# Kernel optimization log

Measured on AMD Instinct MI355X. Metric: run time of the kernel, lower is better.

Reference implementation:

```python
import jax, jax.numpy as jnp
import numpy as np

N = 100000
E = 1600000
E_OUT = 400000
IN_DIM = 16
HID = 64
OUT_DIM = 2
L = 6
BN_EPS = 1e-5


def setup_inputs() -> dict:
    key = jax.random.key(0)
    ks = jax.random.split(key, 12)
    x = jax.random.normal(ks[0], (N, IN_DIM), dtype=jnp.float32)
    edge_index = jax.random.randint(ks[1], (2, E), 0, N, dtype=jnp.int64)
    edge_index_out = jax.random.randint(ks[2], (2, E_OUT), 0, N, dtype=jnp.int64)
    s_emb = 1.0 / np.sqrt(IN_DIM)
    s_hid = 1.0 / np.sqrt(HID)
    W_emb = jax.random.uniform(ks[3], (IN_DIM, HID), jnp.float32, -s_emb, s_emb)
    b_emb = jax.random.uniform(ks[4], (HID,), jnp.float32, -s_emb, s_emb)
    conv_W = jax.random.uniform(ks[5], (L, HID, HID), jnp.float32, -s_hid, s_hid)
    conv_b = jnp.zeros((L, HID), jnp.float32)
    bn_gamma = jnp.ones((L, HID), jnp.float32)
    bn_beta = jnp.zeros((L, HID), jnp.float32)
    s_fc = 1.0 / np.sqrt(2 * HID)
    fc_W = jax.random.uniform(ks[6], (2 * HID, OUT_DIM), jnp.float32, -s_fc, s_fc)
    fc_b = jax.random.uniform(ks[7], (OUT_DIM,), jnp.float32, -s_fc, s_fc)
    return dict(x=x, edge_index=edge_index, edge_index_out=edge_index_out,
                W_emb=W_emb, b_emb=b_emb, conv_W=conv_W, conv_b=conv_b,
                bn_gamma=bn_gamma, bn_beta=bn_beta, fc_W=fc_W, fc_b=fc_b)


def gcn_conv(h, W, b, src, dst, norm):
    # PyG GCNConv: h' = scatter_add(norm * (hW)[src] -> dst) + b
    hw = h @ W                                   # [N, HID]
    msgs = hw[src] * norm[:, None]               # [E+N, HID] gather
    agg = jax.ops.segment_sum(msgs, dst, num_segments=N)
    return agg + b


def batchnorm_train(h, gamma, beta):
    mean = jnp.mean(h, axis=0)
    var = jnp.mean(jnp.square(h - mean), axis=0)  # biased var (BN training)
    return (h - mean) * jax.lax.rsqrt(var + BN_EPS) * gamma + beta


def reference(x, edge_index, edge_index_out, W_emb, b_emb, conv_W, conv_b,
              bn_gamma, bn_beta, fc_W, fc_b):
    # add self-loops + symmetric normalization (computed once, shared by layers)
    loop = jnp.arange(N, dtype=edge_index.dtype)
    src = jnp.concatenate([edge_index[0], loop])
    dst = jnp.concatenate([edge_index[1], loop])
    deg = jax.ops.segment_sum(jnp.ones_like(dst, dtype=jnp.float32), dst, num_segments=N)
    dinv = jnp.where(deg > 0, jax.lax.rsqrt(jnp.maximum(deg, 1.0)), 0.0)
    norm = dinv[src] * dinv[dst]

    x_embed = x @ W_emb + b_emb                  # node embedding [N, HID]
    for i in range(L):
        h = gcn_conv(x_embed, conv_W[i], conv_b[i], src, dst, norm)
        h = jax.nn.relu(batchnorm_train(h, bn_gamma[i], bn_beta[i]))
        x_embed = x_embed + h                    # residual

    e_src, e_dst = edge_index_out[0], edge_index_out[1]
    edge_repr = jnp.concatenate([x_embed[e_src], x_embed[e_dst]], axis=-1)  # [E_out, 2*HID]
    return edge_repr @ fc_W + fc_b
```

## Files before the change

kernel.cpp:

```cpp
#include <hip/hip_runtime.h>

#define NN 100000
#define NE 1600000
#define NEO 400000
#define HID 64
#define NL 6
#define BN_EPS 1e-5f

#define SPMM_BLOCKS 6250
#define SCAN_BS 512
#define SCAN_NB 196
#define GRP_ROWS 12500

#define BIN_CHUNK 1024
#define BIN_J (BIN_CHUNK / 256)
#define BIN_BLOCKS ((NE + BIN_CHUNK - 1) / BIN_CHUNK)
#define BIN_CAP 210000
#define B2_BPG 98
#define H2_BPG 98

#define OFF_ECOL 0
#define OFF_XE   NE
#define OFF_AGG  (OFF_XE + NN * 32)
#define OFF_HWB  (OFF_AGG + NN * 32)

#define OD_DINV   0
#define OD_ROWPTR 100352
#define OD_CC     200704
#define OD_BSUM   300704
#define OD_SS     300960
#define OD_SUMS   301088
#define OD_GCUR   309280

typedef __attribute__((ext_vector_type(8))) short bf16x8;
typedef __attribute__((ext_vector_type(4))) float f32x4;

static __device__ __forceinline__ unsigned short f2bf(float f) {
    unsigned u = __float_as_uint(f);
    unsigned r = (u + 0x7FFF + ((u >> 16) & 1)) >> 16;
    return (unsigned short)r;
}
static __device__ __forceinline__ float bflo(unsigned u) {
    return __uint_as_float(u << 16);
}
static __device__ __forceinline__ float bfhi(unsigned u) {
    return __uint_as_float(u & 0xFFFF0000u);
}

__global__ void k_bin(const int* __restrict__ src, const int* __restrict__ dst,
                      int* __restrict__ gcur,
                      int* __restrict__ bsrc, int* __restrict__ bdst) {
    __shared__ int cw[4][8], bw[4][8], ow[4][8];
    int t = threadIdx.x;
    int w = t >> 6;
    if (t < 32) { ((int*)cw)[t] = 0; ((int*)ow)[t] = 0; }
    __syncthreads();
    int cb = blockIdx.x * BIN_CHUNK;
    int s[BIN_J], d[BIN_J], g[BIN_J];
#pragma unroll
    for (int j = 0; j < BIN_J; j++) {
        int e = cb + t + j * 256;
        s[j] = (e < NE) ? src[e] : -1;
        d[j] = (e < NE) ? dst[e] : -1;
        if (d[j] >= 0) {
            g[j] = (unsigned)d[j] / GRP_ROWS;
            atomicAdd(&cw[w][g[j]], 1);
        }
    }
    __syncthreads();
    if (t < 8) {
        int c0 = cw[0][t], c1 = cw[1][t], c2 = cw[2][t], c3 = cw[3][t];
        int base = t * BIN_CAP + atomicAdd(&gcur[t], c0 + c1 + c2 + c3);
        bw[0][t] = base;
        bw[1][t] = base + c0;
        bw[2][t] = base + c0 + c1;
        bw[3][t] = base + c0 + c1 + c2;
    }
    __syncthreads();
#pragma unroll
    for (int j = 0; j < BIN_J; j++) {
        if (d[j] >= 0) {
            int pos = bw[w][g[j]] + atomicAdd(&ow[w][g[j]], 1);
            bsrc[pos] = s[j];
            bdst[pos] = d[j];
        }
    }
}

__global__ void k_hist2(const int* __restrict__ gcur, const int* __restrict__ bdst,
                        int* __restrict__ cnt) {
    int g = blockIdx.x & 7;
    int b = blockIdx.x >> 3;
    int n = gcur[g];
    int base = g * BIN_CAP;
    for (int i = b * blockDim.x + threadIdx.x; i < n; i += H2_BPG * blockDim.x)
        atomicAdd(&cnt[bdst[base + i]], 1);
}

__global__ void k_scanA(const int* __restrict__ cnt, int* __restrict__ rowptr,
                        int* __restrict__ bsum, float* __restrict__ dinv) {
    __shared__ int sh[SCAN_BS];
    int t = threadIdx.x;
    int i = blockIdx.x * SCAN_BS + t;
    int v = (i < NN) ? cnt[i] : 0;
    sh[t] = v;
    __syncthreads();
    for (int off = 1; off < SCAN_BS; off <<= 1) {
        int a = (t >= off) ? sh[t - off] : 0;
        __syncthreads();
        sh[t] += a;
        __syncthreads();
    }
    if (i < NN) {
        rowptr[i] = sh[t] - v;
        dinv[i] = rsqrtf((float)(v + 1));
    }
    if (t == SCAN_BS - 1) bsum[blockIdx.x] = sh[t];
}

__global__ void k_scanB(int* __restrict__ bsum) {
    __shared__ int sh[256];
    int t = threadIdx.x;
    int v = (t < SCAN_NB) ? bsum[t] : 0;
    sh[t] = v;
    __syncthreads();
    for (int off = 1; off < 256; off <<= 1) {
        int a = (t >= off) ? sh[t - off] : 0;
        __syncthreads();
        sh[t] += a;
        __syncthreads();
    }
    if (t < SCAN_NB) bsum[t] = (t == 0) ? 0 : sh[t - 1];
}

__global__ void k_scanC(int* __restrict__ rowptr, const int* __restrict__ bsum,
                        int* __restrict__ cursor) {
    int i = blockIdx.x * SCAN_BS + threadIdx.x;
    if (i < NN) {
        int rp = rowptr[i] + bsum[blockIdx.x];
        rowptr[i] = rp;
        cursor[i] = rp;
    }
    if (i == 0) rowptr[NN] = NE;
}

__global__ void k_build2(const int* __restrict__ gcur, const int* __restrict__ bsrc,
                         const int* __restrict__ bdst, int* __restrict__ cursor,
                         int* __restrict__ ecol) {
    int g = blockIdx.x & 7;
    int b = blockIdx.x >> 3;
    int n = gcur[g];
    int base = g * BIN_CAP;
    for (int i = b * blockDim.x + threadIdx.x; i < n; i += B2_BPG * blockDim.x) {
        int d = bdst[base + i];
        int s = bsrc[base + i];
        int pos = atomicAdd(&cursor[d], 1);
        ecol[pos] = s;
    }
}

__global__ void k_embed(const float* __restrict__ x, const float* __restrict__ W,
                        const float* __restrict__ b, unsigned short* __restrict__ xe16) {
    __shared__ float Ws[16 * 64];
    __shared__ float bs[64];
    int t = threadIdx.x;
    for (int i = t; i < 16 * 64; i += 256) Ws[i] = W[i];
    if (t < 64) bs[t] = b[t];
    __syncthreads();
    int c = t & 63, r = t >> 6;
    int n0 = blockIdx.x * 64;
    for (int n = n0 + r; n < n0 + 64 && n < NN; n += 4) {
        const float* xr = x + n * 16;
        float acc = bs[c];
#pragma unroll
        for (int k = 0; k < 16; k++) acc = fmaf(xr[k], Ws[k * 64 + c], acc);
        xe16[(size_t)n * 64 + c] = f2bf(acc);
    }
}

__global__ void k_hw(unsigned short* __restrict__ xe16,
                     const float* __restrict__ W, const float* __restrict__ dinv,
                     const unsigned short* __restrict__ agg16,
                     const float* __restrict__ gamma, const float* __restrict__ beta,
                     const double* __restrict__ sumsPrev, double* __restrict__ sumsCur,
                     unsigned short* __restrict__ hwb, int apply) {
    __shared__ unsigned short Wt[64 * 72];
    __shared__ unsigned short Xb[64 * 72];
    __shared__ float sss[128];
    int t = threadIdx.x;
    int n0 = blockIdx.x * 64;
    if (blockIdx.x == 0) {
        for (int i = t; i < 2048; i += 256) sumsCur[i] = 0.0;
    }
    if (apply && t < 64) {
        double s = 0.0, q = 0.0;
#pragma unroll
        for (int k = 0; k < 16; k++) {
            s += sumsPrev[k * 128 + t];
            q += sumsPrev[k * 128 + 64 + t];
        }
        double mean = s / (double)NN;
        double var = q / (double)NN - mean * mean;
        float sc = gamma[t] * rsqrtf((float)var + BN_EPS);
        sss[t] = sc;
        sss[64 + t] = beta[t] - (float)mean * sc;
    }

    {
        int c = t & 63, r = t >> 6;
#pragma unroll
        for (int jj = 0; jj < 4; jj++) {
            float w0 = W[(r * 16 + jj * 4 + 0) * 64 + c];
            float w1 = W[(r * 16 + jj * 4 + 1) * 64 + c];
            float w2 = W[(r * 16 + jj * 4 + 2) * 64 + c];
            float w3 = W[(r * 16 + jj * 4 + 3) * 64 + c];
            uint2 pk;
            pk.x = ((unsigned)f2bf(w1) << 16) | f2bf(w0);
            pk.y = ((unsigned)f2bf(w3) << 16) | f2bf(w2);
            *(uint2*)&Wt[c * 72 + r * 16 + jj * 4] = pk;
        }
    }
    __syncthreads();

    {
        int n = t >> 2, kq = t & 3;
        int node = n0 + n;
        unsigned xs[8] = {0, 0, 0, 0, 0, 0, 0, 0};
        if (node < NN) {
            const uint4* xr = (const uint4*)(xe16 + (size_t)node * 64 + kq * 16);
            uint4 x0 = xr[0], x1 = xr[1];
            xs[0] = x0.x; xs[1] = x0.y; xs[2] = x0.z; xs[3] = x0.w;
            xs[4] = x1.x; xs[5] = x1.y; xs[6] = x1.z; xs[7] = x1.w;
            if (apply) {
                const uint4* ar = (const uint4*)(agg16 + (size_t)node * 64 + kq * 16);
                uint4 a0 = ar[0], a1 = ar[1];
                unsigned as[8] = {a0.x, a0.y, a0.z, a0.w, a1.x, a1.y, a1.z, a1.w};
                int c = kq * 16;
#pragma unroll
                for (int i = 0; i < 8; i++) {
                    float v0 = bflo(xs[i]) +
                               fmaxf(fmaf(bflo(as[i]), sss[c + 2 * i], sss[64 + c + 2 * i]), 0.f);
                    float v1 = bfhi(xs[i]) +
                               fmaxf(fmaf(bfhi(as[i]), sss[c + 2 * i + 1], sss[64 + c + 2 * i + 1]), 0.f);
                    xs[i] = ((unsigned)f2bf(v1) << 16) | f2bf(v0);
                }
                uint4* xw = (uint4*)(xe16 + (size_t)node * 64 + kq * 16);
                xw[0] = make_uint4(xs[0], xs[1], xs[2], xs[3]);
                xw[1] = make_uint4(xs[4], xs[5], xs[6], xs[7]);
            }
        }
        *(uint4*)&Xb[n * 72 + kq * 16] = make_uint4(xs[0], xs[1], xs[2], xs[3]);
        *(uint4*)&Xb[n * 72 + kq * 16 + 8] = make_uint4(xs[4], xs[5], xs[6], xs[7]);
    }
    __syncthreads();

    int lane = t & 63, w = t >> 6;
    int m = lane & 15, quad = lane >> 4;
    f32x4 acc[4];
#pragma unroll
    for (int tc = 0; tc < 4; tc++) acc[tc] = (f32x4){0.f, 0.f, 0.f, 0.f};
#pragma unroll
    for (int s = 0; s < 2; s++) {
        bf16x8 bfr = *(const bf16x8*)&Xb[(w * 16 + m) * 72 + s * 32 + quad * 8];
#pragma unroll
        for (int tc = 0; tc < 4; tc++) {
            bf16x8 afr = *(const bf16x8*)&Wt[(tc * 16 + m) * 72 + s * 32 + quad * 8];
            acc[tc] = __builtin_amdgcn_mfma_f32_16x16x32_bf16(afr, bfr, acc[tc], 0, 0, 0);
        }
    }
    int node = n0 + w * 16 + m;
    if (node < NN) {
        float di = dinv[node];
#pragma unroll
        for (int tc = 0; tc < 4; tc++) {
            int c0 = tc * 16 + quad * 4;
            uint2 pk;
            pk.x = ((unsigned)f2bf(acc[tc][1] * di) << 16) | f2bf(acc[tc][0] * di);
            pk.y = ((unsigned)f2bf(acc[tc][3] * di) << 16) | f2bf(acc[tc][2] * di);
            *(uint2*)(hwb + (size_t)node * 64 + c0) = pk;
        }
    }
}

__global__ void k_spmm(const int* __restrict__ rowptr, const int* __restrict__ ecol,
                       const unsigned short* __restrict__ hwb, const float* __restrict__ dinv,
                       unsigned short* __restrict__ agg16, double* __restrict__ sums) {
    int t = threadIdx.x;
    int w = t >> 6, l = t & 63;
    int r = l >> 4;
    int sub = (l >> 3) & 1;
    int q = l & 7;
    const uint4* hw4 = (const uint4*)hwb;
    float ls[8], lq[8];
#pragma unroll
    for (int j = 0; j < 8; j++) { ls[j] = 0.f; lq[j] = 0.f; }
    for (int row0 = blockIdx.x * 16 + w * 4; row0 < NN; row0 += SPMM_BLOCKS * 16) {
        int row = row0 + r;
        bool valid = row < NN;
        int p0 = 0, p1 = 0;
        float a[8];
#pragma unroll
        for (int j = 0; j < 8; j++) a[j] = 0.f;
        if (valid) {
            p0 = rowptr[row];
            p1 = rowptr[row + 1];
            if (sub == 0) {
                uint4 sv = hw4[(size_t)row * 8 + q];
                a[0] = bflo(sv.x); a[1] = bfhi(sv.x); a[2] = bflo(sv.y); a[3] = bfhi(sv.y);
                a[4] = bflo(sv.z); a[5] = bfhi(sv.z); a[6] = bflo(sv.w); a[7] = bfhi(sv.w);
            }
        }
        int p = p0 + sub;
        for (; p + 2 < p1; p += 4) {
            int s0 = ecol[p], s1 = ecol[p + 2];
            uint4 u0 = hw4[(size_t)s0 * 8 + q];
            uint4 u1 = hw4[(size_t)s1 * 8 + q];
            a[0] += bflo(u0.x); a[1] += bfhi(u0.x); a[2] += bflo(u0.y); a[3] += bfhi(u0.y);
            a[4] += bflo(u0.z); a[5] += bfhi(u0.z); a[6] += bflo(u0.w); a[7] += bfhi(u0.w);
            a[0] += bflo(u1.x); a[1] += bfhi(u1.x); a[2] += bflo(u1.y); a[3] += bfhi(u1.y);
            a[4] += bflo(u1.z); a[5] += bfhi(u1.z); a[6] += bflo(u1.w); a[7] += bfhi(u1.w);
        }
        if (p < p1) {
            int s0 = ecol[p];
            uint4 u0 = hw4[(size_t)s0 * 8 + q];
            a[0] += bflo(u0.x); a[1] += bfhi(u0.x); a[2] += bflo(u0.y); a[3] += bfhi(u0.y);
            a[4] += bflo(u0.z); a[5] += bfhi(u0.z); a[6] += bflo(u0.w); a[7] += bfhi(u0.w);
        }
#pragma unroll
        for (int j = 0; j < 8; j++) a[j] += __shfl_xor(a[j], 8, 64);
        if (valid && sub == 0) {
            float di = dinv[row];
            unsigned pk[4];
#pragma unroll
            for (int j = 0; j < 4; j++) {
                float v0 = a[2 * j] * di, v1 = a[2 * j + 1] * di;
                pk[j] = ((unsigned)f2bf(v1) << 16) | f2bf(v0);
            }
            *(uint4*)(agg16 + (size_t)row * 64 + 8 * q) = make_uint4(pk[0], pk[1], pk[2], pk[3]);
#pragma unroll
            for (int j = 0; j < 4; j++) {
                float v0 = bflo(pk[j]), v1 = bfhi(pk[j]);
                ls[2 * j] += v0; ls[2 * j + 1] += v1;
                lq[2 * j] = fmaf(v0, v0, lq[2 * j]);
                lq[2 * j + 1] = fmaf(v1, v1, lq[2 * j + 1]);
            }
        }
    }
#pragma unroll
    for (int j = 0; j < 8; j++) {
        ls[j] += __shfl_xor(ls[j], 16, 64); ls[j] += __shfl_xor(ls[j], 32, 64);
        lq[j] += __shfl_xor(lq[j], 16, 64); lq[j] += __shfl_xor(lq[j], 32, 64);
    }
    __shared__ float Ss[4][64], Sq[4][64];
    if (l < 8) {
#pragma unroll
        for (int j = 0; j < 8; j++) {
            Ss[w][8 * l + j] = ls[j];
            Sq[w][8 * l + j] = lq[j];
        }
    }
    __syncthreads();
    if (t < 64) {
        float a = Ss[0][t] + Ss[1][t] + Ss[2][t] + Ss[3][t];
        float b = Sq[0][t] + Sq[1][t] + Sq[2][t] + Sq[3][t];
        double* sh = sums + (blockIdx.x & 15) * 128;
        atomicAdd(&sh[t], (double)a);
        atomicAdd(&sh[64 + t], (double)b);
    }
}

__global__ void k_finalize(const double* __restrict__ sums, const float* __restrict__ gamma,
                           const float* __restrict__ beta, float* __restrict__ ss) {
    int c = threadIdx.x;
    double s = 0.0, q = 0.0;
#pragma unroll
    for (int k = 0; k < 16; k++) { s += sums[k * 128 + c]; q += sums[k * 128 + 64 + c]; }
    double mean = s / (double)NN;
    double var = q / (double)NN - mean * mean;
    float sc = gamma[c] * rsqrtf((float)var + BN_EPS);
    ss[c] = sc;
    ss[64 + c] = beta[c] - (float)mean * sc;
}

__global__ void k_apply(const unsigned short* __restrict__ agg16, const float* __restrict__ ss,
                        unsigned short* __restrict__ xe16) {
    int i = blockIdx.x * blockDim.x + threadIdx.x;
    if (i < NN * 8) {
        int c0 = (i & 7) * 8;
        uint4 av = *(const uint4*)(agg16 + (size_t)i * 8);
        uint4 xv = *(const uint4*)(xe16 + (size_t)i * 8);
        unsigned as[4] = {av.x, av.y, av.z, av.w};
        unsigned xs[4] = {xv.x, xv.y, xv.z, xv.w};
#pragma unroll
        for (int j = 0; j < 4; j++) {
            int c = c0 + 2 * j;
            float v0 = bflo(xs[j]) + fmaxf(fmaf(bflo(as[j]), ss[c], ss[64 + c]), 0.f);
            float v1 = bfhi(xs[j]) + fmaxf(fmaf(bfhi(as[j]), ss[c + 1], ss[64 + c + 1]), 0.f);
            xs[j] = ((unsigned)f2bf(v1) << 16) | f2bf(v0);
        }
        *(uint4*)(xe16 + (size_t)i * 8) = make_uint4(xs[0], xs[1], xs[2], xs[3]);
    }
}

__global__ void k_out(const int* __restrict__ esrc, const int* __restrict__ edst,
                      const unsigned short* __restrict__ xe16, const float* __restrict__ fcW,
                      const float* __restrict__ fcb, float* __restrict__ out) {
    __shared__ float Ws[256];
    __shared__ float bs[2];
    int t = threadIdx.x;
    for (int i = t; i < 256; i += 256) Ws[i] = fcW[i];
    if (t < 2) bs[t] = fcb[t];
    __syncthreads();
    int e = blockIdx.x * blockDim.x + t;
    if (e < NEO) {
        int s = esrc[e], d = edst[e];
        const uint4* rs = (const uint4*)(xe16 + (size_t)s * 64);
        const uint4* rd = (const uint4*)(xe16 + (size_t)d * 64);
        float a0 = bs[0], a1 = bs[1];
#pragma unroll
        for (int i = 0; i < 8; i++) {
            uint4 v = rs[i];
            int c = i * 8;
            a0 += bflo(v.x) * Ws[(c + 0) * 2] + bfhi(v.x) * Ws[(c + 1) * 2] +
                  bflo(v.y) * Ws[(c + 2) * 2] + bfhi(v.y) * Ws[(c + 3) * 2] +
                  bflo(v.z) * Ws[(c + 4) * 2] + bfhi(v.z) * Ws[(c + 5) * 2] +
                  bflo(v.w) * Ws[(c + 6) * 2] + bfhi(v.w) * Ws[(c + 7) * 2];
            a1 += bflo(v.x) * Ws[(c + 0) * 2 + 1] + bfhi(v.x) * Ws[(c + 1) * 2 + 1] +
                  bflo(v.y) * Ws[(c + 2) * 2 + 1] + bfhi(v.y) * Ws[(c + 3) * 2 + 1] +
                  bflo(v.z) * Ws[(c + 4) * 2 + 1] + bfhi(v.z) * Ws[(c + 5) * 2 + 1] +
                  bflo(v.w) * Ws[(c + 6) * 2 + 1] + bfhi(v.w) * Ws[(c + 7) * 2 + 1];
        }
#pragma unroll
        for (int i = 0; i < 8; i++) {
            uint4 v = rd[i];
            int c = 64 + i * 8;
            a0 += bflo(v.x) * Ws[(c + 0) * 2] + bfhi(v.x) * Ws[(c + 1) * 2] +
                  bflo(v.y) * Ws[(c + 2) * 2] + bfhi(v.y) * Ws[(c + 3) * 2] +
                  bflo(v.z) * Ws[(c + 4) * 2] + bfhi(v.z) * Ws[(c + 5) * 2] +
                  bflo(v.w) * Ws[(c + 6) * 2] + bfhi(v.w) * Ws[(c + 7) * 2];
            a1 += bflo(v.x) * Ws[(c + 0) * 2 + 1] + bfhi(v.x) * Ws[(c + 1) * 2 + 1] +
                  bflo(v.y) * Ws[(c + 2) * 2 + 1] + bfhi(v.y) * Ws[(c + 3) * 2 + 1] +
                  bflo(v.z) * Ws[(c + 4) * 2 + 1] + bfhi(v.z) * Ws[(c + 5) * 2 + 1] +
                  bflo(v.w) * Ws[(c + 6) * 2 + 1] + bfhi(v.w) * Ws[(c + 7) * 2 + 1];
        }
        out[e * 2] = a0;
        out[e * 2 + 1] = a1;
    }
}

extern "C" void kernel_launch(void* const* d_in, const int* in_sizes, int n_in,
                              void* d_out, int out_size, void* d_ws, size_t ws_size,
                              hipStream_t stream) {
    const float* x      = (const float*)d_in[0];
    const int*   ei     = (const int*)d_in[1];
    const int*   eio    = (const int*)d_in[2];
    const float* W_emb  = (const float*)d_in[3];
    const float* b_emb  = (const float*)d_in[4];
    const float* conv_W = (const float*)d_in[5];
    const float* bn_g   = (const float*)d_in[7];
    const float* bn_b   = (const float*)d_in[8];
    const float* fc_W   = (const float*)d_in[9];
    const float* fc_b   = (const float*)d_in[10];
    float* out = (float*)d_out;

    float* ws   = (float*)d_ws;
    int*   ecol = (int*)(ws + OFF_ECOL);
    unsigned short* xe16  = (unsigned short*)(ws + OFF_XE);
    unsigned short* agg16 = (unsigned short*)(ws + OFF_AGG);
    unsigned short* hwb   = (unsigned short*)(ws + OFF_HWB);
    int* bsrc = (int*)(ws + OFF_XE);
    int* bdst = (int*)(ws + OFF_AGG);

    float* od     = (float*)d_out;
    float* dinv   = od + OD_DINV;
    int*   rowptr = (int*)(od + OD_ROWPTR);
    int*   cc     = (int*)(od + OD_CC);
    int*   bsum   = (int*)(od + OD_BSUM);
    float* ss     = od + OD_SS;
    double* sums  = (double*)(od + OD_SUMS);
    int*   gcur   = (int*)(od + OD_GCUR);

    const int* src  = ei;
    const int* dst  = ei + NE;
    const int* esrc = eio;
    const int* edst = eio + NEO;

    (void)hipMemsetAsync(cc, 0, NN * sizeof(int), stream);
    (void)hipMemsetAsync(gcur, 0, 8 * sizeof(int), stream);
    k_bin<<<BIN_BLOCKS, 256, 0, stream>>>(src, dst, gcur, bsrc, bdst);
    k_hist2<<<8 * H2_BPG, 256, 0, stream>>>(gcur, bdst, cc);
    k_scanA<<<SCAN_NB, SCAN_BS, 0, stream>>>(cc, rowptr, bsum, dinv);
    k_scanB<<<1, 256, 0, stream>>>(bsum);
    k_scanC<<<SCAN_NB, SCAN_BS, 0, stream>>>(rowptr, bsum, cc);
    k_build2<<<8 * B2_BPG, 256, 0, stream>>>(gcur, bsrc, bdst, cc, ecol);

    k_embed<<<(NN + 63) / 64, 256, 0, stream>>>(x, W_emb, b_emb, xe16);

    for (int l = 0; l < NL; l++) {
        double* sumsPrev = sums + ((l + 1) & 1) * 2048;
        double* sumsCur  = sums + (l & 1) * 2048;
        k_hw<<<(NN + 63) / 64, 256, 0, stream>>>(xe16, conv_W + l * 64 * 64, dinv, agg16,
                                                 bn_g + (l ? (l - 1) * 64 : 0),
                                                 bn_b + (l ? (l - 1) * 64 : 0),
                                                 sumsPrev, sumsCur, hwb, l > 0 ? 1 : 0);
        k_spmm<<<SPMM_BLOCKS, 256, 0, stream>>>(rowptr, ecol, hwb, dinv, agg16, sumsCur);
    }
    k_finalize<<<1, 64, 0, stream>>>(sums + ((NL - 1) & 1) * 2048,
                                     bn_g + (NL - 1) * 64, bn_b + (NL - 1) * 64, ss);
    k_apply<<<(NN * 8 + 255) / 256, 256, 0, stream>>>(agg16, ss, xe16);

    k_out<<<(NEO + 255) / 256, 256, 0, stream>>>(esrc, edst, xe16, fc_W, fc_b, out);
}
```

Baseline: 601.3 us.

## Build CSR with two-level radix binning and per-bucket shared-memory counting sort

Replaces the global-atomic histogram, three-kernel scan and global-atomic scatter CSR build with a second binning pass into 256 sub-buckets of 391 rows each. A single 256-entry scan then gives bucket offsets, and each bucket is counting-sorted in LDS to write rowptr, dinv and ecol. Source and local row are packed into one int to halve bin traffic. The aim is to cut global atomics and kernel launches, at the risk of fixed sub-bucket capacity (SBCAP) overflow and a serial per-block prefix loop.

```diff
diff --git a/kernel.cpp b/kernel.cpp
--- a/kernel.cpp
+++ b/kernel.cpp
@@ -8,16 +8,17 @@
 #define BN_EPS 1e-5f
 
 #define SPMM_BLOCKS 6250
-#define SCAN_BS 512
-#define SCAN_NB 196
 #define GRP_ROWS 12500
 
+#define B1CAP 210000
 #define BIN_CHUNK 1024
 #define BIN_J (BIN_CHUNK / 256)
 #define BIN_BLOCKS ((NE + BIN_CHUNK - 1) / BIN_CHUNK)
-#define BIN_CAP 210000
-#define B2_BPG 98
-#define H2_BPG 98
+#define SB_PER_G 32
+#define SB_ROWS 391
+#define SBCAP 7600
+#define BIN2_CHUNK 2048
+#define BIN2_BPG 103
 
 #define OFF_ECOL 0
 #define OFF_XE   NE
@@ -26,11 +27,11 @@
 
 #define OD_DINV   0
 #define OD_ROWPTR 100352
-#define OD_CC     200704
-#define OD_BSUM   300704
 #define OD_SS     300960
 #define OD_SUMS   301088
 #define OD_GCUR   309280
+#define OD_SCNT   309312
+#define OD_SBASE  309568
 
 typedef __attribute__((ext_vector_type(8))) short bf16x8;
 typedef __attribute__((ext_vector_type(4))) float f32x4;
@@ -48,29 +49,30 @@
 }
 
 __global__ void k_bin(const int* __restrict__ src, const int* __restrict__ dst,
-                      int* __restrict__ gcur,
-                      int* __restrict__ bsrc, int* __restrict__ bdst) {
+                      int* __restrict__ gcur, int* __restrict__ b1) {
     __shared__ int cw[4][8], bw[4][8], ow[4][8];
     int t = threadIdx.x;
     int w = t >> 6;
     if (t < 32) { ((int*)cw)[t] = 0; ((int*)ow)[t] = 0; }
     __syncthreads();
     int cb = blockIdx.x * BIN_CHUNK;
-    int s[BIN_J], d[BIN_J], g[BIN_J];
+    int p[BIN_J], g[BIN_J];
 #pragma unroll
     for (int j = 0; j < BIN_J; j++) {
         int e = cb + t + j * 256;
-        s[j] = (e < NE) ? src[e] : -1;
-        d[j] = (e < NE) ? dst[e] : -1;
-        if (d[j] >= 0) {
-            g[j] = (unsigned)d[j] / GRP_ROWS;
+        if (e < NE) {
+            int s = src[e], d = dst[e];
+            g[j] = (unsigned)d / GRP_ROWS;
+            p[j] = (s << 14) | (d - g[j] * GRP_ROWS);
             atomicAdd(&cw[w][g[j]], 1);
+        } else {
+            g[j] = -1;
         }
     }
     __syncthreads();
     if (t < 8) {
         int c0 = cw[0][t], c1 = cw[1][t], c2 = cw[2][t], c3 = cw[3][t];
-        int base = t * BIN_CAP + atomicAdd(&gcur[t], c0 + c1 + c2 + c3);
+        int base = t * B1CAP + atomicAdd(&gcur[t], c0 + c1 + c2 + c3);
         bw[0][t] = base;
         bw[1][t] = base + c0;
         bw[2][t] = base + c0 + c1;
@@ -79,49 +81,62 @@
     __syncthreads();
 #pragma unroll
     for (int j = 0; j < BIN_J; j++) {
-        if (d[j] >= 0) {
+        if (g[j] >= 0) {
             int pos = bw[w][g[j]] + atomicAdd(&ow[w][g[j]], 1);
-            bsrc[pos] = s[j];
-            bdst[pos] = d[j];
-        }
-    }
-}
-
-__global__ void k_hist2(const int* __restrict__ gcur, const int* __restrict__ bdst,
-                        int* __restrict__ cnt) {
+            b1[pos] = p[j];
+        }
+    }
+}
+
+__global__ void k_bin2(const int* __restrict__ gcur, const int* __restrict__ b1,
+                       int* __restrict__ scnt, int* __restrict__ b2) {
+    __shared__ int cw[4][SB_PER_G], bw[4][SB_PER_G], ow[4][SB_PER_G];
+    int t = threadIdx.x;
+    int w = t >> 6;
+    if (t < 128) { ((int*)cw)[t] = 0; ((int*)ow)[t] = 0; }
+    __syncthreads();
     int g = blockIdx.x & 7;
     int b = blockIdx.x >> 3;
     int n = gcur[g];
-    int base = g * BIN_CAP;
-    for (int i = b * blockDim.x + threadIdx.x; i < n; i += H2_BPG * blockDim.x)
-        atomicAdd(&cnt[bdst[base + i]], 1);
-}
-
-__global__ void k_scanA(const int* __restrict__ cnt, int* __restrict__ rowptr,
-                        int* __restrict__ bsum, float* __restrict__ dinv) {
-    __shared__ int sh[SCAN_BS];
-    int t = threadIdx.x;
-    int i = blockIdx.x * SCAN_BS + t;
-    int v = (i < NN) ? cnt[i] : 0;
-    sh[t] = v;
-    __syncthreads();
-    for (int off = 1; off < SCAN_BS; off <<= 1) {
-        int a = (t >= off) ? sh[t - off] : 0;
-        __syncthreads();
-        sh[t] += a;
-        __syncthreads();
-    }
-    if (i < NN) {
-        rowptr[i] = sh[t] - v;
-        dinv[i] = rsqrtf((float)(v + 1));
-    }
-    if (t == SCAN_BS - 1) bsum[blockIdx.x] = sh[t];
-}
-
-__global__ void k_scanB(int* __restrict__ bsum) {
+    const int* in = b1 + g * B1CAP;
+    int c0 = b * BIN2_CHUNK;
+    int p[8], sb[8];
+#pragma unroll
+    for (int j = 0; j < 8; j++) {
+        int e = c0 + t + j * 256;
+        if (e < n) {
+            int v = in[e];
+            int lr = v & 16383;
+            sb[j] = (unsigned)lr / SB_ROWS;
+            p[j] = ((v >> 14) << 9) | (lr - sb[j] * SB_ROWS);
+            atomicAdd(&cw[w][sb[j]], 1);
+        } else {
+            sb[j] = -1;
+        }
+    }
+    __syncthreads();
+    if (t < SB_PER_G) {
+        int a0 = cw[0][t], a1 = cw[1][t], a2 = cw[2][t], a3 = cw[3][t];
+        int base = atomicAdd(&scnt[g * SB_PER_G + t], a0 + a1 + a2 + a3);
+        bw[0][t] = base;
+        bw[1][t] = base + a0;
+        bw[2][t] = base + a0 + a1;
+        bw[3][t] = base + a0 + a1 + a2;
+    }
+    __syncthreads();
+#pragma unroll
+    for (int j = 0; j < 8; j++) {
+        if (sb[j] >= 0) {
+            int pos = bw[w][sb[j]] + atomicAdd(&ow[w][sb[j]], 1);
+            b2[(g * SB_PER_G + sb[j]) * SBCAP + pos] = p[j];
+        }
+    }
+}
+
+__global__ void k_scan256(const int* __restrict__ scnt, int* __restrict__ sbase) {
     __shared__ int sh[256];
     int t = threadIdx.x;
-    int v = (t < SCAN_NB) ? bsum[t] : 0;
+    int v = scnt[t];
     sh[t] = v;
     __syncthreads();
     for (int off = 1; off < 256; off <<= 1) {
@@ -130,33 +145,55 @@
         sh[t] += a;
         __syncthreads();
     }
-    if (t < SCAN_NB) bsum[t] = (t == 0) ? 0 : sh[t - 1];
-}
-
-__global__ void k_scanC(int* __restrict__ rowptr, const int* __restrict__ bsum,
-                        int* __restrict__ cursor) {
-    int i = blockIdx.x * SCAN_BS + threadIdx.x;
-    if (i < NN) {
-        int rp = rowptr[i] + bsum[blockIdx.x];
-        rowptr[i] = rp;
-        cursor[i] = rp;
-    }
-    if (i == 0) rowptr[NN] = NE;
-}
-
-__global__ void k_build2(const int* __restrict__ gcur, const int* __restrict__ bsrc,
-                         const int* __restrict__ bdst, int* __restrict__ cursor,
-                         int* __restrict__ ecol) {
-    int g = blockIdx.x & 7;
-    int b = blockIdx.x >> 3;
-    int n = gcur[g];
-    int base = g * BIN_CAP;
-    for (int i = b * blockDim.x + threadIdx.x; i < n; i += B2_BPG * blockDim.x) {
-        int d = bdst[base + i];
-        int s = bsrc[base + i];
-        int pos = atomicAdd(&cursor[d], 1);
-        ecol[pos] = s;
-    }
+    sbase[t] = sh[t] - v;
+}
+
+__global__ void __launch_bounds__(256) k_build3(
+        const int* __restrict__ scnt, const int* __restrict__ sbase,
+        const int* __restrict__ b2, int* __restrict__ ecol,
+        int* __restrict__ rowptr, float* __restrict__ dinv) {
+    __shared__ int hist[SB_ROWS + 1];
+    __shared__ int lofs[SB_ROWS + 1];
+    __shared__ int lsrc[SBCAP];
+    __shared__ int lout[SBCAP];
+    int sb = blockIdx.x;
+    int g = sb >> 5, sbl = sb & 31;
+    int t = threadIdx.x;
+    int n = scnt[sb];
+    int base = sbase[sb];
+    const int* in = b2 + sb * SBCAP;
+    int row0 = g * GRP_ROWS + sbl * SB_ROWS;
+    int nrows = GRP_ROWS - sbl * SB_ROWS;
+    if (nrows > SB_ROWS) nrows = SB_ROWS;
+    for (int i = t; i < nrows; i += 256) hist[i] = 0;
+    __syncthreads();
+    for (int i = t; i < n; i += 256) {
+        int v = in[i];
+        lsrc[i] = v;
+        atomicAdd(&hist[v & 511], 1);
+    }
+    __syncthreads();
+    if (t == 0) {
+        int acc = 0;
+        for (int r = 0; r < nrows; r++) { lofs[r] = acc; acc += hist[r]; }
+        lofs[nrows] = acc;
+    }
+    __syncthreads();
+    for (int r = t; r < nrows; r += 256) {
+        rowptr[row0 + r] = base + lofs[r];
+        dinv[row0 + r] = rsqrtf((float)(hist[r] + 1));
+    }
+    if (sb == 255 && t == 0) rowptr[NN] = base + n;
+    __syncthreads();
+    for (int r = t; r < nrows; r += 256) hist[r] = lofs[r];
+    __syncthreads();
+    for (int i = t; i < n; i += 256) {
+        int v = lsrc[i];
+        int pos = atomicAdd(&hist[v & 511], 1);
+        lout[pos] = v >> 9;
+    }
+    __syncthreads();
+    for (int i = t; i < n; i += 256) ecol[base + i] = lout[i];
 }
 
 __global__ void k_embed(const float* __restrict__ x, const float* __restrict__ W,
@@ -468,31 +505,29 @@
     unsigned short* xe16  = (unsigned short*)(ws + OFF_XE);
     unsigned short* agg16 = (unsigned short*)(ws + OFF_AGG);
     unsigned short* hwb   = (unsigned short*)(ws + OFF_HWB);
-    int* bsrc = (int*)(ws + OFF_XE);
-    int* bdst = (int*)(ws + OFF_AGG);
+    int* b1 = (int*)(ws + OFF_XE);
+    int* b2 = (int*)(ws + OFF_AGG);
 
     float* od     = (float*)d_out;
     float* dinv   = od + OD_DINV;
     int*   rowptr = (int*)(od + OD_ROWPTR);
-    int*   cc     = (int*)(od + OD_CC);
-    int*   bsum   = (int*)(od + OD_BSUM);
     float* ss     = od + OD_SS;
     double* sums  = (double*)(od + OD_SUMS);
     int*   gcur   = (int*)(od + OD_GCUR);
+    int*   scnt   = (int*)(od + OD_SCNT);
+    int*   sbase  = (int*)(od + OD_SBASE);
 
     const int* src  = ei;
     const int* dst  = ei + NE;
     const int* esrc = eio;
     const int* edst = eio + NEO;
 
-    (void)hipMemsetAsync(cc, 0, NN * sizeof(int), stream);
     (void)hipMemsetAsync(gcur, 0, 8 * sizeof(int), stream);
-    k_bin<<<BIN_BLOCKS, 256, 0, stream>>>(src, dst, gcur, bsrc, bdst);
-    k_hist2<<<8 * H2_BPG, 256, 0, stream>>>(gcur, bdst, cc);
-    k_scanA<<<SCAN_NB, SCAN_BS, 0, stream>>>(cc, rowptr, bsum, dinv);
-    k_scanB<<<1, 256, 0, stream>>>(bsum);
-    k_scanC<<<SCAN_NB, SCAN_BS, 0, stream>>>(rowptr, bsum, cc);
-    k_build2<<<8 * B2_BPG, 256, 0, stream>>>(gcur, bsrc, bdst, cc, ecol);
+    (void)hipMemsetAsync(scnt, 0, 256 * sizeof(int), stream);
+    k_bin<<<BIN_BLOCKS, 256, 0, stream>>>(src, dst, gcur, b1);
+    k_bin2<<<8 * BIN2_BPG, 256, 0, stream>>>(gcur, b1, scnt, b2);
+    k_scan256<<<1, 256, 0, stream>>>(scnt, sbase);
+    k_build3<<<256, 256, 0, stream>>>(scnt, sbase, b2, ecol, rowptr, dinv);
 
     k_embed<<<(NN + 63) / 64, 256, 0, stream>>>(x, W_emb, b_emb, xe16);
 
```

Measured after the change: 486.1 us. -19.2%, faster.
